# Optimization experiments

Hardware: AMD Instinct MI355X
Metric: run time of the kernel (lower is better)

The kernel has to match this reference:

```python
import jax, jax.numpy as jnp
import numpy as np

B, D = 64, 11                 # trees, tree depth
T = 2 ** D - 1                # 2047 nodes per perfect binary tree (heap layout)
H, E, L, V = 256, 256, 5, 50000
LEAF_START = 2 ** (D - 1) - 1 # first leaf index within a tree
N = B * T


def setup_inputs() -> dict:
    key = jax.random.key(0)
    ks = jax.random.split(key, 8)
    wordid = jax.random.randint(ks[0], (N, L), 0, V, dtype=jnp.int32)
    # subtoken mask: 1 for leaf nodes (which carry tokens), 0 for internal nodes
    node_is_leaf = (jnp.arange(T) >= LEAF_START).astype(jnp.int32)      # [T]
    mask = jnp.tile(node_is_leaf[:, None], (B, L))                       # [N, L]
    h0 = jnp.zeros((N, H), jnp.float32)   # init_hidden -> zeros
    c0 = jnp.zeros((N, H), jnp.float32)
    list_root_index = jnp.zeros((B,), jnp.int32)          # root at offset 0 per tree
    list_num_node = jnp.full((B,), T, dtype=jnp.int32)
    s = 0.02
    emb_table = s * jax.random.normal(ks[1], (V, E), jnp.float32)
    W_iou = s * jax.random.normal(ks[2], (3 * H, E), jnp.float32)
    U_iou = s * jax.random.normal(ks[3], (3 * H, 2 * H), jnp.float32)
    b_iou = jnp.zeros((3 * H,), jnp.float32)
    U_f_w = s * jax.random.normal(ks[4], (2 * H, 2 * H), jnp.float32)
    U_f_b = jnp.zeros((2 * H,), jnp.float32)
    return {"wordid": wordid, "mask": mask, "h0": h0, "c0": c0,
            "list_root_index": list_root_index, "list_num_node": list_num_node,
            "emb_table": emb_table, "W_iou": W_iou, "U_iou": U_iou,
            "b_iou": b_iou, "U_f_w": U_f_w, "U_f_b": U_f_b}


def reference(wordid, mask, h0, c0, list_root_index, list_num_node,
              emb_table, W_iou, U_iou, b_iou, U_f_w, U_f_b):
    fm = mask.astype(jnp.float32)
    # tree_leaf_subtoken path: embed masked ids (masked slots hit token 0, as in torch)
    emb = emb_table[wordid * mask]                # [N, L, E]
    wemb = emb.sum(axis=1)                        # [N, E]
    leaf = fm.max(axis=1)                         # [N] node-level mask
    iou0 = (wemb @ W_iou.T) * leaf[:, None]       # [N, 3H] leaf input contribution
    iou0 = iou0.reshape(B, T, 3 * H)
    c0r = c0.reshape(B, T, H)

    def apply_node(iou, c_in):
        i, o, u = jnp.split(iou + b_iou, 3, axis=-1)
        cn = jax.nn.sigmoid(i) * jnp.tanh(u) + c_in
        return jax.nn.sigmoid(o) * jnp.tanh(cn), cn

    h = jnp.zeros((B, T, H), jnp.float32)
    c = jnp.zeros((B, T, H), jnp.float32)

    # frontier 0: leaves (no in-edges -> reduce never fires, c stays c0)
    hl, cl = apply_node(iou0[:, LEAF_START:], c0r[:, LEAF_START:])
    h = h.at[:, LEAF_START:].set(hl)
    c = c.at[:, LEAF_START:].set(cl)

    # topological propagation, level by level bottom-up
    for d in range(D - 2, -1, -1):
        s, e = 2 ** d - 1, 2 ** (d + 1) - 1
        n = e - s
        # children of nodes [s,e) are contiguous at [e, e+2n) as pairs (2i+1, 2i+2)
        h_cat = h[:, e:e + 2 * n].reshape(B, n, 2 * H)
        f = jax.nn.sigmoid(h_cat @ U_f_w.T + U_f_b).reshape(B, n, 2, H)
        c_red = (f * c[:, e:e + 2 * n].reshape(B, n, 2, H)).sum(axis=2)
        iou = h_cat @ U_iou.T                     # reduce_func REPLACES iou (DGL semantics)
        hn, cn = apply_node(iou, c_red)
        h = h.at[:, s:e].set(hn)
        c = c.at[:, s:e].set(cn)

    # all trees have T nodes -> padded tree_output is just h
    tree_output = h                               # [B, T, H]
    root_h, root_c = h[:, 0], c[:, 0]             # list_root_index == 0
    return tree_output, (root_h, root_c)
```

## Files before the change

### kernel.cpp

```cpp
#include <hip/hip_runtime.h>
#include <math.h>

typedef long long i64;
typedef short short8v __attribute__((ext_vector_type(8)));
typedef float float4v __attribute__((ext_vector_type(4)));

#define Hd 256
#define Bb 64
#define Tn 2047
#define LEAF0 1023
#define NTH 33538048LL

__device__ __forceinline__ float frcp(float x){ return __builtin_amdgcn_rcpf(x); }
__device__ __forceinline__ float sigm(float x){ return frcp(1.0f+__expf(-x)); }
__device__ __forceinline__ float ftanh(float x){ return 1.0f - 2.0f*frcp(__expf(2.0f*x)+1.0f); }
__device__ __forceinline__ float bf2f(unsigned short s){
  union { unsigned u; float f; } v; v.u = ((unsigned)s)<<16; return v.f; }
__device__ __forceinline__ short f2bf(float f){
  union { float f; unsigned u; } v; v.f = f;
  unsigned r = v.u + 0x7FFF + ((v.u>>16)&1);
  return (short)(r>>16); }

#define GL2LDS(gp, lp) __builtin_amdgcn_global_load_lds( \
  (const __attribute__((address_space(1))) void*)(gp), \
  (__attribute__((address_space(3))) void*)(lp), 16, 0, 0)

__global__ __launch_bounds__(256)
void prep_kernel(const float* __restrict__ W_iou, const float* __restrict__ U_iou,
                 const float* __restrict__ U_f_w,
                 short* __restrict__ Wt2I, short* __restrict__ Wt2L,
                 const int* __restrict__ wordid, const float* __restrict__ emb,
                 short* __restrict__ hb, short* __restrict__ cbb){
  if (blockIdx.x < 320){
    int t = blockIdx.x*256 + threadIdx.x;
    int lane = t & 63, rest = t >> 6;
    int nr = rest % 20; int rest2 = rest / 20;
    int kt = rest2 & 15, hhb = rest2 >> 4;
    int g = nr/5, strip = nr - g*5;
    int j = strip*256 + hhb*64 + g*16 + (lane&15);
    int k0 = kt*32 + (lane>>4)*8;
    const float* src = (j < 768) ? (U_iou + (i64)j*512 + k0)
                                 : (U_f_w + (i64)(j-768)*512 + k0);
    short* dst = Wt2I + (i64)t*8;
    #pragma unroll
    for (int e=0;e<8;e++) dst[e] = f2bf(src[e]);
  } else if (blockIdx.x < 416){
    int t2 = (blockIdx.x-320)*256 + threadIdx.x;
    int lane = t2 & 63, rest = t2 >> 6;
    int nr = rest % 12; int rest2 = rest / 12;
    int kt = rest2 & 7, hhb = rest2 >> 3;
    int g = nr/3, strip = nr - g*3;
    int j = strip*256 + hhb*64 + g*16 + (lane&15);
    int k0 = kt*32 + (lane>>4)*8;
    const float* src = W_iou + (i64)j*256 + k0;
    short* dst = Wt2L + (i64)t2*8;
    #pragma unroll
    for (int e=0;e<8;e++) dst[e] = f2bf(src[e]);
  } else {
    int id = (blockIdx.x-416)*256 + threadIdx.x;
    int row = id >> 5, q = id & 31;
    int b = row >> 10, j = row & 1023;
    i64 tb = (i64)b*Tn;
    const int* wid = wordid + (tb + LEAF0 + j)*5;
    float s[8];
    #pragma unroll
    for (int e=0;e<8;e++) s[e] = 0.f;
    #pragma unroll
    for (int l=0;l<5;l++){
      const float* er = emb + (i64)wid[l]*Hd + q*8;
      float4 v0 = *(const float4*)(er);
      float4 v1 = *(const float4*)(er+4);
      s[0]+=v0.x; s[1]+=v0.y; s[2]+=v0.z; s[3]+=v0.w;
      s[4]+=v1.x; s[5]+=v1.y; s[6]+=v1.z; s[7]+=v1.w;
    }
    short o[8];
    #pragma unroll
    for (int e=0;e<8;e++) o[e] = f2bf(s[e]);
    short* dst = (j < 1023) ? (hb + (tb + j)*Hd) : (cbb + tb*Hd);
    *(short8v*)(dst + q*8) = *(short8v*)o;
  }
}

__global__ __launch_bounds__(256)
void leaf_gemm(const short* __restrict__ hb, const short* __restrict__ cbb,
               const short* __restrict__ WB,
               const float* __restrict__ b_iou, const float* __restrict__ c0,
               float* __restrict__ hOut, short* __restrict__ hbOut,
               short* __restrict__ cbbOut){
  __shared__ __align__(16) short As[2][4*512];
  const int tid = threadIdx.x;
  const int lane = tid & 63, w = tid >> 6;
  const int bid = blockIdx.x;
  const int hhb = bid & 3;
  const int m0 = (bid >> 2) * 64;

  const int rA = m0 + w*16 + (lane&15);
  const int bA = rA >> 10, jA = rA & 1023;
  const short* baseA = (jA < 1023) ? (hb + ((i64)bA*Tn + jA)*Hd)
                                   : (cbb + (i64)bA*Tn*Hd);
  const short* srcA = baseA + (lane>>4)*8;
  const short* gB0 = WB + (i64)hhb*96*512 + (i64)(w*3)*512 + lane*8;

  float4v acc[4][3];
  #pragma unroll
  for (int mr=0;mr<4;mr++)
    #pragma unroll
    for (int s=0;s<3;s++){ float4v z = {0.f,0.f,0.f,0.f}; acc[mr][s] = z; }

  GL2LDS(srcA, &As[0][w*512]);
  #pragma unroll 2
  for (int kt=0; kt<8; ++kt){
    __syncthreads();
    if (kt+1 < 8) GL2LDS(srcA + (kt+1)*32, &As[(kt+1)&1][w*512]);
    const short* bp = gB0 + (i64)kt*12*512;
    short8v bfr[3];
    #pragma unroll
    for (int s=0;s<3;s++) bfr[s] = *(const short8v*)(bp + (i64)s*512);
    #pragma unroll
    for (int mr=0;mr<4;mr++){
      short8v a = *(const short8v*)&As[kt&1][mr*512 + lane*8];
      #pragma unroll
      for (int s=0;s<3;s++)
        acc[mr][s] = __builtin_amdgcn_mfma_f32_16x16x32_bf16(a, bfr[s], acc[mr][s], 0, 0, 0);
    }
  }

  const int hcol = hhb*64 + w*16 + (lane&15);
  const float bi = b_iou[hcol], bo = b_iou[256+hcol], bu = b_iou[512+hcol];
  #pragma unroll
  for (int mr=0;mr<4;mr++){
    const int mgb = m0 + mr*16 + ((lane>>4)<<2);
    #pragma unroll
    for (int r=0;r<4;r++){
      const int m = mgb + r;
      const int b = m >> 10, j = m & 1023;
      const i64 n = (i64)b*Tn + LEAF0 + j;
      const float i_ = acc[mr][0][r] + bi;
      const float o_ = acc[mr][1][r] + bo;
      const float u_ = acc[mr][2][r] + bu;
      const float cn = sigm(i_)*ftanh(u_) + c0[n*Hd + hcol];
      const float hv = sigm(o_)*ftanh(cn);
      cbbOut[n*Hd + hcol] = f2bf(cn);
      hbOut[n*Hd + hcol]  = f2bf(hv);
      hOut[n*Hd + hcol] = hv;
    }
  }
}

__global__ __launch_bounds__(256)
void level_gemm(const short* __restrict__ WB,
                const float* __restrict__ b_iou, const float* __restrict__ U_f_b,
                float* __restrict__ hOut, short* __restrict__ hb, short* __restrict__ cbb,
                int s0, int e0, int logn){
  __shared__ __align__(16) short As[2][4*512];
  const int tid = threadIdx.x;
  const int lane = tid & 63, w = tid >> 6;
  const int bid = blockIdx.x;
  const int hhb = bid & 3;
  const int m0 = (bid >> 2) * 64;
  const int nm1 = (1<<logn)-1;

  const int rA = m0 + w*16 + (lane&15);
  const int bA = rA >> logn, jA = rA & nm1;
  const short* srcA = hb + ((i64)bA*Tn + e0)*Hd + (i64)jA*512 + (lane>>4)*8;
  const short* gB0 = WB + (i64)hhb*320*512 + (i64)(w*5)*512 + lane*8;

  float4v acc[4][5];
  #pragma unroll
  for (int mr=0;mr<4;mr++)
    #pragma unroll
    for (int s=0;s<5;s++){ float4v z = {0.f,0.f,0.f,0.f}; acc[mr][s] = z; }

  GL2LDS(srcA, &As[0][w*512]);
  #pragma unroll 2
  for (int kt=0; kt<16; ++kt){
    __syncthreads();
    if (kt+1 < 16) GL2LDS(srcA + (kt+1)*32, &As[(kt+1)&1][w*512]);
    const short* bp = gB0 + (i64)kt*20*512;
    short8v bfr[5];
    #pragma unroll
    for (int s=0;s<5;s++) bfr[s] = *(const short8v*)(bp + (i64)s*512);
    #pragma unroll
    for (int mr=0;mr<4;mr++){
      short8v a = *(const short8v*)&As[kt&1][mr*512 + lane*8];
      #pragma unroll
      for (int s=0;s<5;s++)
        acc[mr][s] = __builtin_amdgcn_mfma_f32_16x16x32_bf16(a, bfr[s], acc[mr][s], 0, 0, 0);
    }
  }

  const int hcol = hhb*64 + w*16 + (lane&15);
  const float bi = b_iou[hcol], bo = b_iou[256+hcol], bu = b_iou[512+hcol];
  const float bfl = U_f_b[hcol], bfr2 = U_f_b[256+hcol];
  #pragma unroll
  for (int mr=0;mr<4;mr++){
    const int mgb = m0 + mr*16 + ((lane>>4)<<2);
    #pragma unroll
    for (int r=0;r<4;r++){
      const int m = mgb + r;
      const int b = m >> logn, j = m & nm1;
      const i64 base = (i64)b*Tn;
      const i64 cidx = (base + e0 + 2*j)*Hd + hcol;
      const float cl = bf2f((unsigned short)cbb[cidx]);
      const float cr = bf2f((unsigned short)cbb[cidx + Hd]);
      const float i_ = acc[mr][0][r]+bi, o_ = acc[mr][1][r]+bo, u_ = acc[mr][2][r]+bu;
      const float fl = acc[mr][3][r]+bfl, fr = acc[mr][4][r]+bfr2;
      const float cn = sigm(i_)*ftanh(u_) + sigm(fl)*cl + sigm(fr)*cr;
      const float hv = sigm(o_)*ftanh(cn);
      const i64 oidx = (base + s0 + j)*Hd + hcol;
      cbb[oidx] = f2bf(cn);
      hb[oidx]  = f2bf(hv);
      hOut[oidx] = hv;
    }
  }
}

__global__ __launch_bounds__(512)
void tree_fused(const short* __restrict__ WB, const float* __restrict__ b_iou,
                const float* __restrict__ U_f_b, float* __restrict__ hOut,
                const short* __restrict__ hb, const short* __restrict__ cbb,
                float* __restrict__ outRoot){
  __shared__ __align__(16) char BUF[96*1024];
  char* bAh = BUF;
  char* bAc = BUF + 32*1024;
  char* bBh = BUF + 64*1024;
  char* bBc = BUF + 80*1024;
  const int tid = threadIdx.x;
  const int lane = tid & 63, w = tid >> 6;
  const int hhb = w >> 1;
  const int g0 = (w & 1) * 2;
  const int b = blockIdx.x;
  const i64 tb = (i64)b*Tn;

  #pragma unroll
  for (int p=0;p<4;p++){
    int idx = p*512 + tid;
    int row = idx >> 5, ch = idx & 31;
    int off = row*512 + ((ch*16) ^ (((row>>1)&7)<<4));
    *(short8v*)(bAh + off) = *(const short8v*)(hb  + (tb + 63 + row)*Hd + ch*8);
    *(short8v*)(bAc + off) = *(const short8v*)(cbb + (tb + 63 + row)*Hd + ch*8);
  }
  __syncthreads();

  char* inH = bAh; char* inC = bAc; char* outH = bBh; char* outC = bBc;

  for (int d = 5; d >= 0; --d){
    const int M = 1<<d, s0v = M-1;
    const int nmf = (d == 5) ? 2 : 1;
    for (int mf = 0; mf < nmf; ++mf){
      const int j = mf*16 + (lane&15);
      const int qq = lane >> 4;
      float4v acc[2][5];
      #pragma unroll
      for (int c=0;c<2;c++)
        #pragma unroll
        for (int s=0;s<5;s++){ float4v z = {0.f,0.f,0.f,0.f}; acc[c][s] = z; }
      #pragma unroll 2
      for (int kt=0; kt<16; ++kt){
        const int crow = 2*j + (kt>>3);
        const int ccolB = ((kt&7)*32 + qq*8)*2;
        short8v a = *(const short8v*)(inH + crow*512 + (ccolB ^ (((crow>>1)&7)<<4)));
        const short* bp = WB + (i64)hhb*163840 + (i64)kt*10240 + (i64)lane*8;
        #pragma unroll
        for (int c=0;c<2;c++)
          #pragma unroll
          for (int s=0;s<5;s++){
            short8v bb = *(const short8v*)(bp + (i64)((g0+c)*5+s)*512);
            acc[c][s] = __builtin_amdgcn_mfma_f32_16x16x32_bf16(a, bb, acc[c][s], 0, 0, 0);
          }
      }
      #pragma unroll
      for (int c=0;c<2;c++){
        const int hcol = hhb*64 + (g0+c)*16 + (lane&15);
        const float bi = b_iou[hcol], bo = b_iou[256+hcol], bu = b_iou[512+hcol];
        const float bfl = U_f_b[hcol], bfr2 = U_f_b[256+hcol];
        #pragma unroll
        for (int r=0;r<4;r++){
          const int row = mf*16 + qq*4 + r;
          if (row < M){
            const int cxor = (hcol*2) ^ ((row&7)<<4);
            const float cl = bf2f(*(const unsigned short*)(inC + row*1024 + cxor));
            const float cr = bf2f(*(const unsigned short*)(inC + row*1024 + 512 + cxor));
            const float i_ = acc[c][0][r]+bi, o_ = acc[c][1][r]+bo, u_ = acc[c][2][r]+bu;
            const float fl = acc[c][3][r]+bfl, fr = acc[c][4][r]+bfr2;
            const float cn = sigm(i_)*ftanh(u_) + sigm(fl)*cl + sigm(fr)*cr;
            const float hv = sigm(o_)*ftanh(cn);
            const int woff = row*512 + ((hcol*2) ^ (((row>>1)&7)<<4));
            *(short*)(outH + woff) = f2bf(hv);
            *(short*)(outC + woff) = f2bf(cn);
            hOut[(tb + s0v + row)*Hd + hcol] = hv;
            if (d == 0){
              outRoot[b*Hd + hcol] = hv;
              outRoot[Bb*Hd + b*Hd + hcol] = cn;
            }
          }
        }
      }
    }
    __syncthreads();
    char* t;
    t = inH; inH = outH; outH = t;
    t = inC; inC = outC; outC = t;
  }
}

extern "C" void kernel_launch(void* const* d_in, const int* in_sizes, int n_in,
                              void* d_out, int out_size, void* d_ws, size_t ws_size,
                              hipStream_t stream){
  const int*   wordid = (const int*)  d_in[0];
  const float* c0     = (const float*)d_in[3];
  const float* emb    = (const float*)d_in[6];
  const float* W_iou  = (const float*)d_in[7];
  const float* U_iou  = (const float*)d_in[8];
  const float* b_iou  = (const float*)d_in[9];
  const float* U_f_w  = (const float*)d_in[10];
  const float* U_f_b  = (const float*)d_in[11];

  float* hOut    = (float*)d_out;
  float* outRoot = hOut + NTH;
  short* cbb  = (short*)d_ws;
  short* hb   = cbb + NTH;
  short* Wt2I = hb + NTH;
  short* Wt2L = Wt2I + 655360;

  hipLaunchKernelGGL(prep_kernel, dim3(8608), dim3(256), 0, stream,
                     W_iou, U_iou, U_f_w, Wt2I, Wt2L, wordid, emb, hb, cbb);
  hipLaunchKernelGGL(leaf_gemm, dim3(4096), dim3(256), 0, stream,
                     hb, cbb, Wt2L, b_iou, c0, hOut, hb, cbb);
  for (int d = 9; d >= 6; --d){
    const int n = 1<<d, s = n-1, e = 2*n-1;
    hipLaunchKernelGGL(level_gemm, dim3(4*n), dim3(256), 0, stream,
                       Wt2I, b_iou, U_f_b, hOut, hb, cbb, s, e, d);
  }
  hipLaunchKernelGGL(tree_fused, dim3(64), dim3(512), 0, stream,
                     Wt2I, b_iou, U_f_b, hOut, hb, cbb, outRoot);
}
```

Measured before the change: 406.4 us.

## Load GEMM operands straight to registers with double buffering, 512-thread blocks

The leaf and level GEMM kernels stop staging the A operand through LDS with global_load_lds and block barriers. Each wave now loads its A and B fragments directly from global memory into register double buffers (even/odd), with the K loop fully unrolled so the next step's loads are in flight during the current MFMAs. Blocks grow to 512 threads covering 128 rows, arranged as 2 row groups by 4 column groups, which halves the grid. This removes barriers and LDS traffic, but each wave now reads more global data per MFMA, and register pressure rises under the new launch bounds.

```diff
diff --git a/kernel.cpp b/kernel.cpp
--- a/kernel.cpp
+++ b/kernel.cpp
@@ -20,10 +20,6 @@
   union { float f; unsigned u; } v; v.f = f;
   unsigned r = v.u + 0x7FFF + ((v.u>>16)&1);
   return (short)(r>>16); }
-
-#define GL2LDS(gp, lp) __builtin_amdgcn_global_load_lds( \
-  (const __attribute__((address_space(1))) void*)(gp), \
-  (__attribute__((address_space(3))) void*)(lp), 16, 0, 0)
 
 __global__ __launch_bounds__(256)
 void prep_kernel(const float* __restrict__ W_iou, const float* __restrict__ U_iou,
@@ -81,25 +77,46 @@
   }
 }
 
-__global__ __launch_bounds__(256)
+#define LEAF_STEP(KT, AC, BC, AN, BN)                                        \
+  {                                                                          \
+    if ((KT)+1 < 8){                                                         \
+      _Pragma("unroll")                                                      \
+      for (int mr=0;mr<4;mr++)                                               \
+        AN[mr] = *(const short8v*)(srcA[mr] + ((KT)+1)*32);                  \
+      const short* bp = wbB + (i64)((KT)+1)*12*512;                          \
+      _Pragma("unroll")                                                      \
+      for (int s=0;s<3;s++) BN[s] = *(const short8v*)(bp + (i64)s*512);      \
+    }                                                                        \
+    _Pragma("unroll")                                                        \
+    for (int mr=0;mr<4;mr++)                                                 \
+      _Pragma("unroll")                                                      \
+      for (int s=0;s<3;s++)                                                  \
+        acc[mr][s] = __builtin_amdgcn_mfma_f32_16x16x32_bf16(AC[mr], BC[s], acc[mr][s], 0, 0, 0); \
+  }
+
+__global__ __launch_bounds__(512, 4)
 void leaf_gemm(const short* __restrict__ hb, const short* __restrict__ cbb,
                const short* __restrict__ WB,
                const float* __restrict__ b_iou, const float* __restrict__ c0,
                float* __restrict__ hOut, short* __restrict__ hbOut,
                short* __restrict__ cbbOut){
-  __shared__ __align__(16) short As[2][4*512];
   const int tid = threadIdx.x;
   const int lane = tid & 63, w = tid >> 6;
+  const int wm = w >> 2, wc = w & 3;
   const int bid = blockIdx.x;
   const int hhb = bid & 3;
-  const int m0 = (bid >> 2) * 64;
-
-  const int rA = m0 + w*16 + (lane&15);
-  const int bA = rA >> 10, jA = rA & 1023;
-  const short* baseA = (jA < 1023) ? (hb + ((i64)bA*Tn + jA)*Hd)
-                                   : (cbb + (i64)bA*Tn*Hd);
-  const short* srcA = baseA + (lane>>4)*8;
-  const short* gB0 = WB + (i64)hhb*96*512 + (i64)(w*3)*512 + lane*8;
+  const int m0 = (bid >> 2) * 128;
+
+  const short* srcA[4];
+  #pragma unroll
+  for (int mr=0;mr<4;mr++){
+    const int rA = m0 + wm*64 + mr*16 + (lane&15);
+    const int bA = rA >> 10, jA = rA & 1023;
+    const short* baseA = (jA < 1023) ? (hb + ((i64)bA*Tn + jA)*Hd)
+                                     : (cbb + (i64)bA*Tn*Hd);
+    srcA[mr] = baseA + (lane>>4)*8;
+  }
+  const short* wbB = WB + (i64)hhb*96*512 + (i64)(wc*3)*512 + lane*8;
 
   float4v acc[4][3];
   #pragma unroll
@@ -107,29 +124,22 @@
     #pragma unroll
     for (int s=0;s<3;s++){ float4v z = {0.f,0.f,0.f,0.f}; acc[mr][s] = z; }
 
-  GL2LDS(srcA, &As[0][w*512]);
-  #pragma unroll 2
-  for (int kt=0; kt<8; ++kt){
-    __syncthreads();
-    if (kt+1 < 8) GL2LDS(srcA + (kt+1)*32, &As[(kt+1)&1][w*512]);
-    const short* bp = gB0 + (i64)kt*12*512;
-    short8v bfr[3];
-    #pragma unroll
-    for (int s=0;s<3;s++) bfr[s] = *(const short8v*)(bp + (i64)s*512);
-    #pragma unroll
-    for (int mr=0;mr<4;mr++){
-      short8v a = *(const short8v*)&As[kt&1][mr*512 + lane*8];
-      #pragma unroll
-      for (int s=0;s<3;s++)
-        acc[mr][s] = __builtin_amdgcn_mfma_f32_16x16x32_bf16(a, bfr[s], acc[mr][s], 0, 0, 0);
-    }
-  }
-
-  const int hcol = hhb*64 + w*16 + (lane&15);
+  short8v aE[4], aO[4], bE[3], bO[3];
+  #pragma unroll
+  for (int mr=0;mr<4;mr++) aE[mr] = *(const short8v*)(srcA[mr]);
+  #pragma unroll
+  for (int s=0;s<3;s++) bE[s] = *(const short8v*)(wbB + (i64)s*512);
+
+  LEAF_STEP(0,aE,bE,aO,bO)  LEAF_STEP(1,aO,bO,aE,bE)
+  LEAF_STEP(2,aE,bE,aO,bO)  LEAF_STEP(3,aO,bO,aE,bE)
+  LEAF_STEP(4,aE,bE,aO,bO)  LEAF_STEP(5,aO,bO,aE,bE)
+  LEAF_STEP(6,aE,bE,aO,bO)  LEAF_STEP(7,aO,bO,aE,bE)
+
+  const int hcol = hhb*64 + wc*16 + (lane&15);
   const float bi = b_iou[hcol], bo = b_iou[256+hcol], bu = b_iou[512+hcol];
   #pragma unroll
   for (int mr=0;mr<4;mr++){
-    const int mgb = m0 + mr*16 + ((lane>>4)<<2);
+    const int mgb = m0 + wm*64 + mr*16 + ((lane>>4)<<2);
     #pragma unroll
     for (int r=0;r<4;r++){
       const int m = mgb + r;
@@ -147,23 +157,44 @@
   }
 }
 
-__global__ __launch_bounds__(256)
+#define LVL_STEP(KT, AC, BC, AN, BN)                                         \
+  {                                                                          \
+    if ((KT)+1 < 16){                                                        \
+      _Pragma("unroll")                                                      \
+      for (int mr=0;mr<4;mr++)                                               \
+        AN[mr] = *(const short8v*)(srcA[mr] + ((KT)+1)*32);                  \
+      const short* bp = wbB + (i64)((KT)+1)*20*512;                          \
+      _Pragma("unroll")                                                      \
+      for (int s=0;s<5;s++) BN[s] = *(const short8v*)(bp + (i64)s*512);      \
+    }                                                                        \
+    _Pragma("unroll")                                                        \
+    for (int mr=0;mr<4;mr++)                                                 \
+      _Pragma("unroll")                                                      \
+      for (int s=0;s<5;s++)                                                  \
+        acc[mr][s] = __builtin_amdgcn_mfma_f32_16x16x32_bf16(AC[mr], BC[s], acc[mr][s], 0, 0, 0); \
+  }
+
+__global__ __launch_bounds__(512, 3)
 void level_gemm(const short* __restrict__ WB,
                 const float* __restrict__ b_iou, const float* __restrict__ U_f_b,
                 float* __restrict__ hOut, short* __restrict__ hb, short* __restrict__ cbb,
                 int s0, int e0, int logn){
-  __shared__ __align__(16) short As[2][4*512];
   const int tid = threadIdx.x;
   const int lane = tid & 63, w = tid >> 6;
+  const int wm = w >> 2, wc = w & 3;
   const int bid = blockIdx.x;
   const int hhb = bid & 3;
-  const int m0 = (bid >> 2) * 64;
+  const int m0 = (bid >> 2) * 128;
   const int nm1 = (1<<logn)-1;
 
-  const int rA = m0 + w*16 + (lane&15);
-  const int bA = rA >> logn, jA = rA & nm1;
-  const short* srcA = hb + ((i64)bA*Tn + e0)*Hd + (i64)jA*512 + (lane>>4)*8;
-  const short* gB0 = WB + (i64)hhb*320*512 + (i64)(w*5)*512 + lane*8;
+  const short* srcA[4];
+  #pragma unroll
+  for (int mr=0;mr<4;mr++){
+    const int rA = m0 + wm*64 + mr*16 + (lane&15);
+    const int bA = rA >> logn, jA = rA & nm1;
+    srcA[mr] = hb + ((i64)bA*Tn + e0)*Hd + (i64)jA*512 + (lane>>4)*8;
+  }
+  const short* wbB = WB + (i64)hhb*320*512 + (i64)(wc*5)*512 + lane*8;
 
   float4v acc[4][5];
   #pragma unroll
@@ -171,30 +202,27 @@
     #pragma unroll
     for (int s=0;s<5;s++){ float4v z = {0.f,0.f,0.f,0.f}; acc[mr][s] = z; }
 
-  GL2LDS(srcA, &As[0][w*512]);
-  #pragma unroll 2
-  for (int kt=0; kt<16; ++kt){
-    __syncthreads();
-    if (kt+1 < 16) GL2LDS(srcA + (kt+1)*32, &As[(kt+1)&1][w*512]);
-    const short* bp = gB0 + (i64)kt*20*512;
-    short8v bfr[5];
-    #pragma unroll
-    for (int s=0;s<5;s++) bfr[s] = *(const short8v*)(bp + (i64)s*512);
-    #pragma unroll
-    for (int mr=0;mr<4;mr++){
-      short8v a = *(const short8v*)&As[kt&1][mr*512 + lane*8];
-      #pragma unroll
-      for (int s=0;s<5;s++)
-        acc[mr][s] = __builtin_amdgcn_mfma_f32_16x16x32_bf16(a, bfr[s], acc[mr][s], 0, 0, 0);
-    }
-  }
-
-  const int hcol = hhb*64 + w*16 + (lane&15);
+  short8v aE[4], aO[4], bE[5], bO[5];
+  #pragma unroll
+  for (int mr=0;mr<4;mr++) aE[mr] = *(const short8v*)(srcA[mr]);
+  #pragma unroll
+  for (int s=0;s<5;s++) bE[s] = *(const short8v*)(wbB + (i64)s*512);
+
+  LVL_STEP( 0,aE,bE,aO,bO)  LVL_STEP( 1,aO,bO,aE,bE)
+  LVL_STEP( 2,aE,bE,aO,bO)  LVL_STEP( 3,aO,bO,aE,bE)
+  LVL_STEP( 4,aE,bE,aO,bO)  LVL_STEP( 5,aO,bO,aE,bE)
+  LVL_STEP( 6,aE,bE,aO,bO)  LVL_STEP( 7,aO,bO,aE,bE)
+  LVL_STEP( 8,aE,bE,aO,bO)  LVL_STEP( 9,aO,bO,aE,bE)
+  LVL_STEP(10,aE,bE,aO,bO)  LVL_STEP(11,aO,bO,aE,bE)
+  LVL_STEP(12,aE,bE,aO,bO)  LVL_STEP(13,aO,bO,aE,bE)
+  LVL_STEP(14,aE,bE,aO,bO)  LVL_STEP(15,aO,bO,aE,bE)
+
+  const int hcol = hhb*64 + wc*16 + (lane&15);
   const float bi = b_iou[hcol], bo = b_iou[256+hcol], bu = b_iou[512+hcol];
   const float bfl = U_f_b[hcol], bfr2 = U_f_b[256+hcol];
   #pragma unroll
   for (int mr=0;mr<4;mr++){
-    const int mgb = m0 + mr*16 + ((lane>>4)<<2);
+    const int mgb = m0 + wm*64 + mr*16 + ((lane>>4)<<2);
     #pragma unroll
     for (int r=0;r<4;r++){
       const int m = mgb + r;
@@ -325,11 +353,12 @@
 
   hipLaunchKernelGGL(prep_kernel, dim3(8608), dim3(256), 0, stream,
                      W_iou, U_iou, U_f_w, Wt2I, Wt2L, wordid, emb, hb, cbb);
-  hipLaunchKernelGGL(leaf_gemm, dim3(4096), dim3(256), 0, stream,
+  hipLaunchKernelGGL(leaf_gemm, dim3(2048), dim3(512), 0, stream,
                      hb, cbb, Wt2L, b_iou, c0, hOut, hb, cbb);
   for (int d = 9; d >= 6; --d){
-    const int n = 1<<d, s = n-1, e = 2*n-1;
-    hipLaunchKernelGGL(level_gemm, dim3(4*n), dim3(256), 0, stream,
+    const int n = 1<<d;
+    const int s = n-1, e = 2*n-1;
+    hipLaunchKernelGGL(level_gemm, dim3(2*n), dim3(512), 0, stream,
                        Wt2I, b_iou, U_f_b, hOut, hb, cbb, s, e, d);
   }
   hipLaunchKernelGGL(tree_fused, dim3(64), dim3(512), 0, stream,
```

Result: slower. 527.1 us (+29.7%).
